# Optimization experiments

Measured on AMD Instinct MI355X. Metric: run time of the kernel, lower is better.

## Reference

```python
import jax, jax.numpy as jnp
import numpy as np

DIM = 256          # channels
HEADS = 8
KS = 3             # kernel_size
DIL = (1, 2, 3, 4) # dilation rates
ND = len(DIL)
HEAD_DIM = DIM // HEADS
SCALE = HEAD_DIM ** -0.5
DPG = DIM // ND    # channels per dilation group
EPS = 1e-5


def setup_inputs() -> dict:
    key = jax.random.key(0)
    ks = jax.random.split(key, 4)
    B, H, W = 8, 64, 64
    vi = jax.random.normal(ks[0], (B, DIM, H, W), jnp.float32)
    ir = jax.random.normal(ks[1], (B, DIM, H, W), jnp.float32)
    w_qkv = jax.random.normal(ks[2], (3 * DIM, DIM), jnp.float32) * 0.02  # 1x1 conv, no bias (qkv_bias=False)
    proj_w = jax.random.normal(ks[3], (DIM, DIM), jnp.float32) * 0.02     # nn.Linear weight
    proj_b = jnp.zeros((DIM,), jnp.float32)
    ln_g = jnp.ones((DIM,), jnp.float32)
    ln_b = jnp.zeros((DIM,), jnp.float32)
    return dict(vi=vi, ir=ir, w_qkv=w_qkv, proj_w=proj_w, proj_b=proj_b, ln_g=ln_g, ln_b=ln_b)


def _unfold(t, dil):
    # t: [B, d, H, W] -> [B, d, KS*KS, H, W], same layout as nn.Unfold(KS, dil, pad=dil*(KS-1)//2)
    B, d, H, W = t.shape
    pad = dil * (KS - 1) // 2
    tp = jnp.pad(t, ((0, 0), (0, 0), (pad, pad), (pad, pad)))
    patches = [tp[:, :, i * dil:i * dil + H, j * dil:j * dil + W]
               for i in range(KS) for j in range(KS)]
    return jnp.stack(patches, axis=2)


def _dilate_attention(q, k, v, dil):
    # q,k,v: [B, d, H, W] with d = DPG; returns [B, H, W, d]
    B, d, H, W = q.shape
    h = d // HEAD_DIM
    N = H * W
    kk = KS * KS
    qf = q.reshape(B, h, HEAD_DIM, N)                      # b h d n
    kf = _unfold(k, dil).reshape(B, h, HEAD_DIM, kk, N)    # b h d k n
    vf = _unfold(v, dil).reshape(B, h, HEAD_DIM, kk, N)
    attn = jax.nn.softmax(jnp.einsum('bhdn,bhdkn->bhnk', qf, kf) * SCALE, axis=-1)
    out = jnp.einsum('bhnk,bhdkn->bhnd', attn, vf)         # b h n d
    return out.transpose(0, 2, 1, 3).reshape(B, H, W, d)   # channel = head*HEAD_DIM + c


def _dilate_block(x, w_qkv, proj_w, proj_b, ln_g, ln_b):
    # x: [B, C, H, W]; DilateBlock: permute -> LN -> MultiDilatelocalAttention -> residual -> permute back
    B, C, H, W = x.shape
    xn = x.transpose(0, 2, 3, 1)                           # B H W C
    mu = jnp.mean(xn, -1, keepdims=True)
    var = jnp.var(xn, -1, keepdims=True)
    xn = (xn - mu) * jax.lax.rsqrt(var + EPS) * ln_g + ln_b
    xc = xn.transpose(0, 3, 1, 2)                          # B C H W
    # 1x1 conv qkv -> [B, 3, ND, DPG, H, W]
    qkv = jnp.einsum('oc,bchw->bohw', w_qkv, xc).reshape(B, 3, ND, DPG, H, W)
    outs = [_dilate_attention(qkv[:, 0, i], qkv[:, 1, i], qkv[:, 2, i], DIL[i])
            for i in range(ND)]                            # each [B, H, W, DPG]
    y = jnp.stack(outs, axis=3).reshape(B, H, W, C)        # channel = dil_idx*DPG + c
    y = y @ proj_w.T + proj_b                              # nn.Linear
    return x + y.transpose(0, 3, 1, 2)                     # residual, back to B C H W


def reference(vi, ir, w_qkv, proj_w, proj_b, ln_g, ln_b):
    sub = vi - ir
    div = _dilate_block(sub, w_qkv, proj_w, proj_b, ln_g, ln_b)
    o = jnp.matmul(vi, div)   # batched [H,W]@[H,W] over (B, C)
    return (o, o)
```

## Files before the change

kernel.cpp:

```cpp
#include <hip/hip_runtime.h>
#include <math.h>

#define B_ 8
#define C_ 256
#define N_ 4096
#define NPOS 32768
#define SCALE_ 0.1767766952966369f
#define EPS_ 1e-5f

typedef __attribute__((ext_vector_type(8))) short bf16x8;
typedef __attribute__((ext_vector_type(8))) unsigned short u16x8;
typedef __attribute__((ext_vector_type(4))) float f32x4;

__device__ __forceinline__ unsigned short f2bf(float f) {
  union { float f; unsigned u; } v; v.f = f;
  unsigned r = v.u + 0x7fff + ((v.u >> 16) & 1);
  return (unsigned short)(r >> 16);
}
__device__ __forceinline__ float bf2f(unsigned short u) {
  union { unsigned u; float f; } v; v.u = ((unsigned)u) << 16; return v.f;
}
__device__ __forceinline__ float blo(unsigned u) {
  union { unsigned u; float f; } v; v.u = u << 16; return v.f;
}
__device__ __forceinline__ float bhi(unsigned u) {
  union { unsigned u; float f; } v; v.u = u & 0xffff0000u; return v.f;
}

#define GLD_LDS16(g, l) \
  __builtin_amdgcn_global_load_lds((const __attribute__((address_space(1))) unsigned int*)(g), \
                                   (__attribute__((address_space(3))) unsigned int*)(l), 16, 0, 0)

__global__ __launch_bounds__(256, 4) void k_stream(
    const float* __restrict__ vi, const float* __restrict__ ir,
    const float* __restrict__ wq, const float* __restrict__ pw,
    unsigned short* __restrict__ wdst,
    unsigned short* __restrict__ subB, unsigned short* __restrict__ viB,
    float2* __restrict__ partials)
{
  int t = threadIdx.x;
  int blk = blockIdx.x;
  if (blk >= 1024) {
    int i4 = (blk - 1024) * 256 + t;
    float4 v = (i4 < 49152) ? ((const float4*)wq)[i4] : ((const float4*)pw)[i4 - 49152];
    ushort4 o;
    o.x = f2bf(v.x); o.y = f2bf(v.y); o.z = f2bf(v.z); o.w = f2bf(v.w);
    ((ushort4*)wdst)[i4] = o;
    return;
  }
  __shared__ float redS[4 * 256], redQ[4 * 256];
  int b = blk >> 7;
  int chunk = (blk >> 4) & 7;
  int pgrp = blk & 15;
  int posq = t & 63;
  int cg = t >> 6;
  int c0 = chunk * 32 + cg * 8;
  int n0 = pgrp * 256 + posq * 4;
  size_t base = ((size_t)b * C_ + c0) * N_ + n0;

  float4 V[8], I[8];
  #pragma unroll
  for (int j = 0; j < 8; ++j) V[j] = *(const float4*)&vi[base + (size_t)j * N_];
  #pragma unroll
  for (int j = 0; j < 8; ++j) I[j] = *(const float4*)&ir[base + (size_t)j * N_];

  float s0 = 0.f, s1 = 0.f, s2 = 0.f, s3 = 0.f;
  float q0 = 0.f, q1 = 0.f, q2 = 0.f, q3 = 0.f;
  #pragma unroll
  for (int j = 0; j < 8; ++j) {
    float4 v4 = V[j], i4 = I[j];
    float4 sv;
    sv.x = v4.x - i4.x; sv.y = v4.y - i4.y; sv.z = v4.z - i4.z; sv.w = v4.w - i4.w;
    ushort4 sb, vb;
    sb.x = f2bf(sv.x); sb.y = f2bf(sv.y); sb.z = f2bf(sv.z); sb.w = f2bf(sv.w);
    vb.x = f2bf(v4.x); vb.y = f2bf(v4.y); vb.z = f2bf(v4.z); vb.w = f2bf(v4.w);
    *(ushort4*)&subB[base + (size_t)j * N_] = sb;
    *(ushort4*)&viB[base + (size_t)j * N_] = vb;
    s0 += sv.x; q0 += sv.x * sv.x;
    s1 += sv.y; q1 += sv.y * sv.y;
    s2 += sv.z; q2 += sv.z * sv.z;
    s3 += sv.w; q3 += sv.w * sv.w;
  }
  *(f32x4*)&redS[cg * 256 + posq * 4] = (f32x4){s0, s1, s2, s3};
  *(f32x4*)&redQ[cg * 256 + posq * 4] = (f32x4){q0, q1, q2, q3};
  __syncthreads();
  float s = redS[t] + redS[256 + t] + redS[512 + t] + redS[768 + t];
  float q = redQ[t] + redQ[256 + t] + redQ[512 + t] + redQ[768 + t];
  partials[(size_t)chunk * NPOS + b * 4096 + pgrp * 256 + t] = make_float2(s, q);
}

__global__ __launch_bounds__(256, 4) void k_lnt(
    const unsigned short* __restrict__ subB,
    const float2* __restrict__ partials,
    const float* __restrict__ ln_g, const float* __restrict__ ln_b,
    unsigned short* __restrict__ xn)
{
  __shared__ __align__(16) unsigned short tile[64 * 256];
  __shared__ float muS[64], rsS[64];
  __shared__ float sG[256], sBt[256];
  int t = threadIdx.x;
  int blk = blockIdx.x;
  int b = blk >> 6, pt = blk & 63;
  int bp0 = b * 4096 + pt * 64;
  sG[t] = ln_g[t];
  sBt[t] = ln_b[t];
  if (t < 64) {
    float s = 0.f, q = 0.f;
    #pragma unroll
    for (int ch = 0; ch < 8; ++ch) {
      float2 pp = partials[(size_t)ch * NPOS + bp0 + t];
      s += pp.x; q += pp.y;
    }
    float mu = s * (1.f / 256.f);
    float var = q * (1.f / 256.f) - mu * mu;
    muS[t] = mu;
    rsS[t] = rsqrtf(var + EPS_);
  }
  int po = t & 7;
  int c = t >> 3;
  u16x8 L[8];
  #pragma unroll
  for (int it = 0; it < 8; ++it) {
    int cc = c + it * 32;
    L[it] = *(const u16x8*)&subB[((size_t)b * C_ + cc) * N_ + pt * 64 + po * 8];
  }
  #pragma unroll
  for (int it = 0; it < 8; ++it) {
    int cs = (c + it * 32) ^ (po << 3);
    #pragma unroll
    for (int e = 0; e < 8; ++e)
      tile[(po * 8 + e) * 256 + cs] = (unsigned short)L[it][e];
  }
  __syncthreads();
  int pos8 = t >> 5;
  int oc = t & 31;
  #pragma unroll
  for (int pass = 0; pass < 8; ++pass) {
    int p = pass * 8 + pos8;
    float mu = muS[p], rs = rsS[p];
    int ocs = oc ^ (p >> 3);
    u16x8 tv = *(const u16x8*)&tile[p * 256 + ocs * 8];
    int c0 = oc * 8;
    u16x8 ov;
    #pragma unroll
    for (int e = 0; e < 8; ++e) {
      float v = bf2f((unsigned short)tv[e]);
      ov[e] = f2bf((v - mu) * rs * sG[c0 + e] + sBt[c0 + e]);
    }
    *(u16x8*)&xn[(size_t)(bp0 + p) * 256 + c0] = ov;
  }
}

template<int EPI, int NT>
__global__ __launch_bounds__(256) void k_gemm_mfma(
    const unsigned short* __restrict__ A,
    const unsigned short* __restrict__ Bw,
    unsigned short* __restrict__ Cout,
    const float* __restrict__ bias,
    const unsigned short* __restrict__ subB,
    int ldc)
{
  __shared__ __align__(16) unsigned short As[128 * 32];
  __shared__ __align__(16) unsigned short Bs[128 * 32];
  __shared__ __align__(16) unsigned short Cs[64 * 136];
  int flat = blockIdx.x;
  int xcd = flat & 7;
  int l = flat >> 3;
  int ml = l / NT;
  int nn = l - ml * NT;
  int m0 = (xcd * 32 + ml) * 128;
  int n0 = nn * 128;
  int tid = threadIdx.x;
  int wv = tid >> 6;
  int lane = tid & 63;
  int mw = (wv >> 1) * 64, nw = (wv & 1) * 64;
  int r = lane & 15, q = lane >> 4;

  int seg0 = wv * 2;
  int srow0 = seg0 * 16 + (lane >> 2);
  int scol = (lane & 3) * 8;
  const unsigned short* ga0 = A  + (size_t)(m0 + srow0) * 256 + scol;
  const unsigned short* ga1 = ga0 + 16 * 256;
  const unsigned short* gb0 = Bw + (size_t)(n0 + srow0) * 256 + scol;
  const unsigned short* gb1 = gb0 + 16 * 256;
  unsigned short* la0 = &As[seg0 * 512];
  unsigned short* la1 = la0 + 512;
  unsigned short* lb0 = &Bs[seg0 * 512];
  unsigned short* lb1 = lb0 + 512;

  f32x4 acc[4][4];
  #pragma unroll
  for (int i = 0; i < 4; ++i)
    #pragma unroll
    for (int j = 0; j < 4; ++j)
      acc[i][j] = (f32x4){0.f, 0.f, 0.f, 0.f};

  for (int k0 = 0; k0 < 256; k0 += 32) {
    GLD_LDS16(ga0 + k0, la0);
    GLD_LDS16(ga1 + k0, la1);
    GLD_LDS16(gb0 + k0, lb0);
    GLD_LDS16(gb1 + k0, lb1);
    __syncthreads();
    bf16x8 af[4], bfr[4];
    #pragma unroll
    for (int mt = 0; mt < 4; ++mt)
      af[mt] = *(const bf16x8*)&As[(mw + mt * 16 + r) * 32 + q * 8];
    #pragma unroll
    for (int nt = 0; nt < 4; ++nt)
      bfr[nt] = *(const bf16x8*)&Bs[(nw + nt * 16 + r) * 32 + q * 8];
    #pragma unroll
    for (int mt = 0; mt < 4; ++mt)
      #pragma unroll
      for (int nt = 0; nt < 4; ++nt)
        acc[mt][nt] = __builtin_amdgcn_mfma_f32_16x16x32_bf16(af[mt], bfr[nt], acc[mt][nt], 0, 0, 0);
    __syncthreads();
  }

  int b = m0 >> 12;
  int nn0 = m0 & 4095;
  #pragma unroll
  for (int pass = 0; pass < 2; ++pass) {
    __syncthreads();
    if (EPI == 0) {
      if ((wv >> 1) == pass) {
        #pragma unroll
        for (int mt = 0; mt < 4; ++mt) {
          int lr = mt * 16 + q * 4;
          #pragma unroll
          for (int nt = 0; nt < 4; ++nt) {
            int col = nw + nt * 16 + r;
            #pragma unroll
            for (int rr = 0; rr < 4; ++rr)
              Cs[(lr + rr) * 136 + col] = f2bf(acc[mt][nt][rr]);
          }
        }
      }
    } else {
      if ((wv & 1) == pass) {
        #pragma unroll
        for (int nt = 0; nt < 4; ++nt) {
          int lr = nt * 16 + r;
          #pragma unroll
          for (int mt = 0; mt < 4; ++mt) {
            int pc = mw + mt * 16 + q * 4;
            #pragma unroll
            for (int rr = 0; rr < 4; ++rr)
              Cs[lr * 136 + pc + rr] = f2bf(acc[mt][nt][rr]);
          }
        }
      }
    }
    __syncthreads();
    if (EPI == 0) {
      #pragma unroll
      for (int cc = 0; cc < 4; ++cc) {
        int ch = cc * 256 + tid;
        int row = ch >> 4, cg = ch & 15;
        u16x8 cv = *(const u16x8*)&Cs[row * 136 + cg * 8];
        int m = m0 + pass * 64 + row;
        *(u16x8*)&Cout[(size_t)m * ldc + n0 + cg * 8] = cv;
      }
    } else {
      #pragma unroll
      for (int cc = 0; cc < 4; ++cc) {
        int ch = cc * 256 + tid;
        int row = ch >> 4, cg = ch & 15;
        u16x8 cv = *(const u16x8*)&Cs[row * 136 + cg * 8];
        int c = n0 + pass * 64 + row;
        size_t idx = ((size_t)(b * 256 + c)) * 4096 + nn0 + cg * 8;
        u16x8 sv = *(const u16x8*)&subB[idx];
        float bb = bias[c];
        u16x8 ov;
        #pragma unroll
        for (int e = 0; e < 8; ++e)
          ov[e] = f2bf(bf2f((unsigned short)cv[e]) + bb + bf2f((unsigned short)sv[e]));
        *(u16x8*)&Cout[idx] = ov;
      }
    }
  }
}

__global__ __launch_bounds__(256) void k_attn(
    const unsigned short* __restrict__ qkv,
    unsigned short* __restrict__ y)
{
  int t = threadIdx.x;
  int sub = t >> 2;
  int lane4 = t & 3;
  int item = blockIdx.x * 64 + sub;
  int ih = item & 7;
  int p = item >> 3;
  int i = ih >> 1, h = ih & 1;
  int dil = i + 1;
  int b = p >> 12;
  int n = p & 4095;
  int py = n >> 6, px = n & 63;
  int off = i * 64 + h * 32 + lane4 * 8;
  const unsigned short* base = qkv + off;

  uint4 qw = *(const uint4*)(base + (size_t)p * 768);
  float q0 = blo(qw.x), q1 = bhi(qw.x), q2 = blo(qw.y), q3 = bhi(qw.y),
        q4 = blo(qw.z), q5 = bhi(qw.z), q6 = blo(qw.w), q7 = bhi(qw.w);

  int pj[9];
  #pragma unroll
  for (int j = 0; j < 9; ++j) {
    int ny = py + (j / 3 - 1) * dil;
    int nx = px + (j % 3 - 1) * dil;
    bool ok = ((unsigned)ny < 64u) && ((unsigned)nx < 64u);
    pj[j] = ok ? ((b << 12) + (ny << 6) + nx) : -1;
  }

  float sc[9];
  #pragma unroll
  for (int j = 0; j < 9; ++j) {
    float s = 0.f;
    if (pj[j] >= 0) {
      uint4 kw = *(const uint4*)(base + 256 + (size_t)pj[j] * 768);
      s  = q0 * blo(kw.x) + q1 * bhi(kw.x);
      s += q2 * blo(kw.y) + q3 * bhi(kw.y);
      s += q4 * blo(kw.z) + q5 * bhi(kw.z);
      s += q6 * blo(kw.w) + q7 * bhi(kw.w);
    }
    s += __shfl_xor(s, 1, 4);
    s += __shfl_xor(s, 2, 4);
    sc[j] = s * SCALE_;
  }

  float mx = sc[0];
  #pragma unroll
  for (int j = 1; j < 9; ++j) mx = fmaxf(mx, sc[j]);
  float e[9], ssum = 0.f;
  #pragma unroll
  for (int j = 0; j < 9; ++j) { e[j] = __expf(sc[j] - mx); ssum += e[j]; }
  float inv = 1.f / ssum;

  float o0 = 0.f, o1 = 0.f, o2 = 0.f, o3 = 0.f, o4 = 0.f, o5 = 0.f, o6 = 0.f, o7 = 0.f;
  #pragma unroll
  for (int j = 0; j < 9; ++j) {
    if (pj[j] >= 0) {
      float w = e[j] * inv;
      uint4 vw = *(const uint4*)(base + 512 + (size_t)pj[j] * 768);
      o0 += w * blo(vw.x); o1 += w * bhi(vw.x);
      o2 += w * blo(vw.y); o3 += w * bhi(vw.y);
      o4 += w * blo(vw.z); o5 += w * bhi(vw.z);
      o6 += w * blo(vw.w); o7 += w * bhi(vw.w);
    }
  }

  u16x8 ov;
  ov[0] = f2bf(o0); ov[1] = f2bf(o1); ov[2] = f2bf(o2); ov[3] = f2bf(o3);
  ov[4] = f2bf(o4); ov[5] = f2bf(o5); ov[6] = f2bf(o6); ov[7] = f2bf(o7);
  *(u16x8*)(y + (size_t)p * 256 + off) = ov;
}

__global__ __launch_bounds__(256) void k_bmm(
    const unsigned short* __restrict__ viB,
    const unsigned short* __restrict__ divmB,
    float* __restrict__ out)
{
  __shared__ __align__(16) unsigned short Vs[64 * 72];
  __shared__ __align__(16) unsigned short Ds[64 * 72];
  int bc = blockIdx.x;
  size_t base = (size_t)bc * 4096;
  int t = threadIdx.x;
  {
    int flat = t * 16;
    int row = flat >> 6, col = flat & 63;
    u16x8 v0 = *(const u16x8*)&viB[base + flat];
    u16x8 v1 = *(const u16x8*)&viB[base + flat + 8];
    *(u16x8*)&Vs[row * 72 + col] = v0;
    *(u16x8*)&Vs[row * 72 + col + 8] = v1;
    u16x8 d0 = *(const u16x8*)&divmB[base + flat];
    u16x8 d1 = *(const u16x8*)&divmB[base + flat + 8];
    #pragma unroll
    for (int e = 0; e < 8; ++e) {
      Ds[(col + e) * 72 + row] = (unsigned short)d0[e];
      Ds[(col + 8 + e) * 72 + row] = (unsigned short)d1[e];
    }
  }
  __syncthreads();
  int w = t >> 6, lane = t & 63;
  int r = lane & 15, q = lane >> 4;
  int wi = (w >> 1) * 32, wj = (w & 1) * 32;
  f32x4 acc[2][2];
  #pragma unroll
  for (int i = 0; i < 2; ++i)
    #pragma unroll
    for (int j = 0; j < 2; ++j)
      acc[i][j] = (f32x4){0.f, 0.f, 0.f, 0.f};
  #pragma unroll
  for (int ks = 0; ks < 2; ++ks) {
    bf16x8 a[2], bfr[2];
    #pragma unroll
    for (int ti = 0; ti < 2; ++ti)
      a[ti] = *(const bf16x8*)&Vs[(wi + ti * 16 + r) * 72 + ks * 32 + q * 8];
    #pragma unroll
    for (int tj = 0; tj < 2; ++tj)
      bfr[tj] = *(const bf16x8*)&Ds[(wj + tj * 16 + r) * 72 + ks * 32 + q * 8];
    #pragma unroll
    for (int ti = 0; ti < 2; ++ti)
      #pragma unroll
      for (int tj = 0; tj < 2; ++tj)
        acc[ti][tj] = __builtin_amdgcn_mfma_f32_16x16x32_bf16(a[ti], bfr[tj], acc[ti][tj], 0, 0, 0);
  }
  #pragma unroll
  for (int ti = 0; ti < 2; ++ti)
    #pragma unroll
    for (int tj = 0; tj < 2; ++tj)
      #pragma unroll
      for (int rr = 0; rr < 4; ++rr) {
        int row = wi + ti * 16 + q * 4 + rr;
        int col = wj + tj * 16 + r;
        float v = acc[ti][tj][rr];
        out[base + row * 64 + col] = v;
        out[8388608ull + base + row * 64 + col] = v;
      }
}

extern "C" void kernel_launch(void* const* d_in, const int* in_sizes, int n_in,
                              void* d_out, int out_size, void* d_ws, size_t ws_size,
                              hipStream_t stream) {
  const float* vi     = (const float*)d_in[0];
  const float* ir     = (const float*)d_in[1];
  const float* w_qkv  = (const float*)d_in[2];
  const float* proj_w = (const float*)d_in[3];
  const float* proj_b = (const float*)d_in[4];
  const float* ln_g   = (const float*)d_in[5];
  const float* ln_b   = (const float*)d_in[6];
  float* out = (float*)d_out;
  char* ws = (char*)d_ws;
  unsigned short* subB = (unsigned short*)(ws);
  unsigned short* qkvb = (unsigned short*)(ws + 16777216);
  float2* partials     = (float2*)(ws + 16777216);
  unsigned short* divmB= (unsigned short*)(ws + 16777216);
  unsigned short* xnb  = (unsigned short*)(ws + 67108864);
  unsigned short* yb   = (unsigned short*)(ws + 83886080);
  unsigned short* viB  = (unsigned short*)(ws + 100663296);
  unsigned short* wqb  = (unsigned short*)(ws + 117440512);
  unsigned short* pwb  = wqb + 196608;

  k_stream<<<1280, 256, 0, stream>>>(vi, ir, w_qkv, proj_w, wqb, subB, viB, partials);
  k_lnt<<<512, 256, 0, stream>>>(subB, partials, ln_g, ln_b, xnb);
  k_gemm_mfma<0, 6><<<1536, 256, 0, stream>>>(xnb, wqb, qkvb, nullptr, nullptr, 768);
  k_attn<<<4096, 256, 0, stream>>>(qkvb, yb);
  k_gemm_mfma<1, 2><<<512, 256, 0, stream>>>(yb, pwb, divmB, proj_b, subB, 0);
  k_bmm<<<2048, 256, 0, stream>>>(viB, divmB, out);
}
```

Baseline: 210.9 us.

## Fold LayerNorm into QKV GEMM epilogue and write position-major sub in stream kernel

Removes the separate LayerNorm/transpose kernel. The stream kernel now writes a position-major bf16 copy of sub through an LDS transpose and also precomputes gamma-scaled QKV weights plus the per-output sums G and Bb. The QKV GEMM runs on the raw un-normalised activations and applies the per-row affine (rs, -mu*rs) and per-column G and Bb terms in its epilogue. This saves a full kernel launch and a read-write pass over the activations, at the cost of extra LDS work in k_stream and some numerical change from normalising after the matmul in bf16.

```diff
diff --git a/kernel.cpp b/kernel.cpp
--- a/kernel.cpp
+++ b/kernel.cpp
@@ -34,24 +34,47 @@
 __global__ __launch_bounds__(256, 4) void k_stream(
     const float* __restrict__ vi, const float* __restrict__ ir,
     const float* __restrict__ wq, const float* __restrict__ pw,
+    const float* __restrict__ ln_g, const float* __restrict__ ln_b,
     unsigned short* __restrict__ wdst,
     unsigned short* __restrict__ subB, unsigned short* __restrict__ viB,
-    float2* __restrict__ partials)
+    unsigned short* __restrict__ xpos,
+    float2* __restrict__ partials, float* __restrict__ Gv, float* __restrict__ Bbv)
 {
   int t = threadIdx.x;
   int blk = blockIdx.x;
-  if (blk >= 1024) {
-    int i4 = (blk - 1024) * 256 + t;
-    float4 v = (i4 < 49152) ? ((const float4*)wq)[i4] : ((const float4*)pw)[i4 - 49152];
+  if (blk < 3) {
+    int o = blk * 256 + t;
+    float g = 0.f, bb = 0.f;
+    #pragma unroll 8
+    for (int c = 0; c < 256; ++c) {
+      float w = wq[o * 256 + c];
+      g += bf2f(f2bf(w * ln_g[c]));
+      bb += w * ln_b[c];
+    }
+    Gv[o] = g; Bbv[o] = bb;
+    return;
+  }
+  if (blk < 259) {
+    int i4 = (blk - 3) * 256 + t;
     ushort4 o;
-    o.x = f2bf(v.x); o.y = f2bf(v.y); o.z = f2bf(v.z); o.w = f2bf(v.w);
+    if (i4 < 49152) {
+      float4 v = ((const float4*)wq)[i4];
+      int c = (i4 << 2) & 255;
+      v.x *= ln_g[c]; v.y *= ln_g[c + 1]; v.z *= ln_g[c + 2]; v.w *= ln_g[c + 3];
+      o.x = f2bf(v.x); o.y = f2bf(v.y); o.z = f2bf(v.z); o.w = f2bf(v.w);
+    } else {
+      float4 v = ((const float4*)pw)[i4 - 49152];
+      o.x = f2bf(v.x); o.y = f2bf(v.y); o.z = f2bf(v.z); o.w = f2bf(v.w);
+    }
     ((ushort4*)wdst)[i4] = o;
     return;
   }
   __shared__ float redS[4 * 256], redQ[4 * 256];
-  int b = blk >> 7;
-  int chunk = (blk >> 4) & 7;
-  int pgrp = blk & 15;
+  __shared__ __align__(16) unsigned short tile2[32 * 264];
+  int sblk = blk - 259;
+  int b = sblk >> 7;
+  int chunk = (sblk >> 4) & 7;
+  int pgrp = sblk & 15;
   int posq = t & 63;
   int cg = t >> 6;
   int c0 = chunk * 32 + cg * 8;
@@ -76,6 +99,7 @@
     vb.x = f2bf(v4.x); vb.y = f2bf(v4.y); vb.z = f2bf(v4.z); vb.w = f2bf(v4.w);
     *(ushort4*)&subB[base + (size_t)j * N_] = sb;
     *(ushort4*)&viB[base + (size_t)j * N_] = vb;
+    *(ushort4*)&tile2[(cg * 8 + j) * 264 + posq * 4] = sb;
     s0 += sv.x; q0 += sv.x * sv.x;
     s1 += sv.y; q1 += sv.y * sv.y;
     s2 += sv.z; q2 += sv.z * sv.z;
@@ -84,70 +108,25 @@
   *(f32x4*)&redS[cg * 256 + posq * 4] = (f32x4){s0, s1, s2, s3};
   *(f32x4*)&redQ[cg * 256 + posq * 4] = (f32x4){q0, q1, q2, q3};
   __syncthreads();
-  float s = redS[t] + redS[256 + t] + redS[512 + t] + redS[768 + t];
-  float q = redQ[t] + redQ[256 + t] + redQ[512 + t] + redQ[768 + t];
-  partials[(size_t)chunk * NPOS + b * 4096 + pgrp * 256 + t] = make_float2(s, q);
-}
-
-__global__ __launch_bounds__(256, 4) void k_lnt(
-    const unsigned short* __restrict__ subB,
-    const float2* __restrict__ partials,
-    const float* __restrict__ ln_g, const float* __restrict__ ln_b,
-    unsigned short* __restrict__ xn)
-{
-  __shared__ __align__(16) unsigned short tile[64 * 256];
-  __shared__ float muS[64], rsS[64];
-  __shared__ float sG[256], sBt[256];
-  int t = threadIdx.x;
-  int blk = blockIdx.x;
-  int b = blk >> 6, pt = blk & 63;
-  int bp0 = b * 4096 + pt * 64;
-  sG[t] = ln_g[t];
-  sBt[t] = ln_b[t];
-  if (t < 64) {
-    float s = 0.f, q = 0.f;
-    #pragma unroll
-    for (int ch = 0; ch < 8; ++ch) {
-      float2 pp = partials[(size_t)ch * NPOS + bp0 + t];
-      s += pp.x; q += pp.y;
-    }
-    float mu = s * (1.f / 256.f);
-    float var = q * (1.f / 256.f) - mu * mu;
-    muS[t] = mu;
-    rsS[t] = rsqrtf(var + EPS_);
-  }
-  int po = t & 7;
-  int c = t >> 3;
-  u16x8 L[8];
-  #pragma unroll
-  for (int it = 0; it < 8; ++it) {
-    int cc = c + it * 32;
-    L[it] = *(const u16x8*)&subB[((size_t)b * C_ + cc) * N_ + pt * 64 + po * 8];
-  }
-  #pragma unroll
-  for (int it = 0; it < 8; ++it) {
-    int cs = (c + it * 32) ^ (po << 3);
-    #pragma unroll
-    for (int e = 0; e < 8; ++e)
-      tile[(po * 8 + e) * 256 + cs] = (unsigned short)L[it][e];
-  }
-  __syncthreads();
-  int pos8 = t >> 5;
-  int oc = t & 31;
-  #pragma unroll
-  for (int pass = 0; pass < 8; ++pass) {
-    int p = pass * 8 + pos8;
-    float mu = muS[p], rs = rsS[p];
-    int ocs = oc ^ (p >> 3);
-    u16x8 tv = *(const u16x8*)&tile[p * 256 + ocs * 8];
-    int c0 = oc * 8;
-    u16x8 ov;
-    #pragma unroll
-    for (int e = 0; e < 8; ++e) {
-      float v = bf2f((unsigned short)tv[e]);
-      ov[e] = f2bf((v - mu) * rs * sG[c0 + e] + sBt[c0 + e]);
-    }
-    *(u16x8*)&xn[(size_t)(bp0 + p) * 256 + c0] = ov;
+  {
+    float s = redS[t] + redS[256 + t] + redS[512 + t] + redS[768 + t];
+    float q = redQ[t] + redQ[256 + t] + redQ[512 + t] + redQ[768 + t];
+    partials[(size_t)chunk * NPOS + b * 4096 + pgrp * 256 + t] = make_float2(s, q);
+  }
+  {
+    u16x8 o0, o1, o2, o3;
+    #pragma unroll
+    for (int wc = 0; wc < 8; ++wc) {
+      o0[wc] = tile2[wc * 264 + t];
+      o1[wc] = tile2[(wc + 8) * 264 + t];
+      o2[wc] = tile2[(wc + 16) * 264 + t];
+      o3[wc] = tile2[(wc + 24) * 264 + t];
+    }
+    size_t xr = ((size_t)b * 4096 + pgrp * 256 + t) * 256 + chunk * 32;
+    *(u16x8*)&xpos[xr] = o0;
+    *(u16x8*)&xpos[xr + 8] = o1;
+    *(u16x8*)&xpos[xr + 16] = o2;
+    *(u16x8*)&xpos[xr + 24] = o3;
   }
 }
 
@@ -158,11 +137,15 @@
     unsigned short* __restrict__ Cout,
     const float* __restrict__ bias,
     const unsigned short* __restrict__ subB,
-    int ldc)
+    int ldc,
+    const float2* __restrict__ partials,
+    const float* __restrict__ Gv,
+    const float* __restrict__ Bbv)
 {
   __shared__ __align__(16) unsigned short As[128 * 32];
   __shared__ __align__(16) unsigned short Bs[128 * 32];
   __shared__ __align__(16) unsigned short Cs[64 * 136];
+  __shared__ float aS[128], bS[128], Gs[128], Bb2[128];
   int flat = blockIdx.x;
   int xcd = flat & 7;
   int l = flat >> 3;
@@ -176,6 +159,25 @@
   int mw = (wv >> 1) * 64, nw = (wv & 1) * 64;
   int r = lane & 15, q = lane >> 4;
 
+  if (EPI == 2) {
+    if (tid < 128) {
+      int p = m0 + tid;
+      float s = 0.f, qq = 0.f;
+      #pragma unroll
+      for (int ch = 0; ch < 8; ++ch) {
+        float2 pp = partials[(size_t)ch * NPOS + p];
+        s += pp.x; qq += pp.y;
+      }
+      float mu = s * (1.f / 256.f);
+      float var = qq * (1.f / 256.f) - mu * mu;
+      float rs = rsqrtf(var + EPS_);
+      aS[tid] = rs;
+      bS[tid] = -mu * rs;
+      Gs[tid] = Gv[n0 + tid];
+      Bb2[tid] = Bbv[n0 + tid];
+    }
+  }
+
   int seg0 = wv * 2;
   int srow0 = seg0 * 16 + (lane >> 2);
   int scol = (lane & 3) * 8;
@@ -221,7 +223,7 @@
   #pragma unroll
   for (int pass = 0; pass < 2; ++pass) {
     __syncthreads();
-    if (EPI == 0) {
+    if (EPI != 1) {
       if ((wv >> 1) == pass) {
         #pragma unroll
         for (int mt = 0; mt < 4; ++mt) {
@@ -230,8 +232,14 @@
           for (int nt = 0; nt < 4; ++nt) {
             int col = nw + nt * 16 + r;
             #pragma unroll
-            for (int rr = 0; rr < 4; ++rr)
-              Cs[(lr + rr) * 136 + col] = f2bf(acc[mt][nt][rr]);
+            for (int rr = 0; rr < 4; ++rr) {
+              float vv = acc[mt][nt][rr];
+              if (EPI == 2) {
+                int mrow = pass * 64 + lr + rr;
+                vv = fmaf(vv, aS[mrow], fmaf(bS[mrow], Gs[col], Bb2[col]));
+              }
+              Cs[(lr + rr) * 136 + col] = f2bf(vv);
+            }
           }
         }
       }
@@ -251,7 +259,7 @@
       }
     }
     __syncthreads();
-    if (EPI == 0) {
+    if (EPI != 1) {
       #pragma unroll
       for (int cc = 0; cc < 4; ++cc) {
         int ch = cc * 256 + tid;
@@ -432,18 +440,22 @@
   char* ws = (char*)d_ws;
   unsigned short* subB = (unsigned short*)(ws);
   unsigned short* qkvb = (unsigned short*)(ws + 16777216);
-  float2* partials     = (float2*)(ws + 16777216);
   unsigned short* divmB= (unsigned short*)(ws + 16777216);
-  unsigned short* xnb  = (unsigned short*)(ws + 67108864);
+  unsigned short* xpos = (unsigned short*)(ws + 67108864);
   unsigned short* yb   = (unsigned short*)(ws + 83886080);
   unsigned short* viB  = (unsigned short*)(ws + 100663296);
   unsigned short* wqb  = (unsigned short*)(ws + 117440512);
   unsigned short* pwb  = wqb + 196608;
-
-  k_stream<<<1280, 256, 0, stream>>>(vi, ir, w_qkv, proj_w, wqb, subB, viB, partials);
-  k_lnt<<<512, 256, 0, stream>>>(subB, partials, ln_g, ln_b, xnb);
-  k_gemm_mfma<0, 6><<<1536, 256, 0, stream>>>(xnb, wqb, qkvb, nullptr, nullptr, 768);
+  float2* partials     = (float2*)(ws + 125829120);
+  float* Gv            = (float*)(ws + 127926272);
+  float* Bbv           = (float*)(ws + 127930368);
+
+  k_stream<<<1283, 256, 0, stream>>>(vi, ir, w_qkv, proj_w, ln_g, ln_b,
+                                     wqb, subB, viB, xpos, partials, Gv, Bbv);
+  k_gemm_mfma<2, 6><<<1536, 256, 0, stream>>>(xpos, wqb, qkvb, nullptr, nullptr, 768,
+                                              partials, Gv, Bbv);
   k_attn<<<4096, 256, 0, stream>>>(qkvb, yb);
-  k_gemm_mfma<1, 2><<<512, 256, 0, stream>>>(yb, pwb, divmB, proj_b, subB, 0);
+  k_gemm_mfma<1, 2><<<512, 256, 0, stream>>>(yb, pwb, divmB, proj_b, subB, 0,
+                                             nullptr, nullptr, nullptr);
   k_bmm<<<2048, 256, 0, stream>>>(viB, divmB, out);
 }
```

New measurement: 225.9 us. 7.1% more time.
